# Kernel optimization log

Hardware: AMD Instinct MI355X
Metric: run time of the kernel (lower is better)

The kernel has to match this reference:

```python
import jax, jax.numpy as jnp
import numpy as np
from jax import lax

EPS = 1e-5

def silu(x):
    return x * jax.nn.sigmoid(x)

def rms_norm(x, w):
    return x * lax.rsqrt(jnp.mean(x * x, axis=-1, keepdims=True) + EPS) * w

def causal_dwconv(x, w, b):
    # x: (B, L, d), w: (d, K) depthwise causal conv, pad left K-1
    K = w.shape[1]
    L = x.shape[1]
    xp = jnp.pad(x, ((0, 0), (K - 1, 0), (0, 0)))
    y = sum(w[:, k] * xp[:, k:k + L, :] for k in range(K))
    return y + b

def selective_scan(xs_in, dt, Bm, Cm, A):
    # xs_in, dt: (B, L, d); Bm, Cm: (B, L, n); A: (d, n)
    Bsz, L, d = xs_in.shape
    n = A.shape[1]

    def step(h, inp):
        dt_t, B_t, C_t, x_t = inp  # (B,d),(B,n),(B,n),(B,d)
        dA = jnp.exp(dt_t[:, :, None] * A)            # (B,d,n)
        h = h * dA + (dt_t * x_t)[:, :, None] * B_t[:, None, :]
        y = jnp.einsum('bdn,bn->bd', h, C_t)
        return h, y

    xs = (jnp.swapaxes(dt, 0, 1), jnp.swapaxes(Bm, 0, 1),
          jnp.swapaxes(Cm, 0, 1), jnp.swapaxes(xs_in, 0, 1))
    h0 = jnp.zeros((Bsz, d, n), xs_in.dtype)
    _, ys = lax.scan(step, h0, xs)
    return jnp.swapaxes(ys, 0, 1)  # (B, L, d)

def mamba1(x, nw, ipw, cw, cb, xpw, dtw, dtb, Alog, Dp, opw):
    # Block: out = mixer(rmsnorm(x)); caller adds residual x.
    xn = rms_norm(x, nw)
    xz = xn @ ipw.T                      # (B,L,2d)
    d = ipw.shape[0] // 2
    xc, z = xz[..., :d], xz[..., d:]
    xc = silu(causal_dwconv(xc, cw, cb))
    dbl = xc @ xpw.T                     # (B,L,r+2n)
    r = dtw.shape[1]
    n = Alog.shape[1]
    dt = jax.nn.softplus(dbl[..., :r] @ dtw.T + dtb)  # (B,L,d)
    Bm = dbl[..., r:r + n]
    Cm = dbl[..., r + n:r + 2 * n]
    A = -jnp.exp(Alog)
    y = selective_scan(xc, dt, Bm, Cm, A)
    y = y + Dp * xc
    y = y * silu(z)
    return y @ opw.T

def mamba_bidir(x, P, i_f, i_b):
    # P: tuple of stacked param arrays; indices select direction-specific params
    (nw, ipw, cw, cb, xpw, dtw, dtb, Alog, Dp, opw) = P

    def m(xx, i):
        return mamba1(xx, nw[i], ipw[i], cw[i], cb[i], xpw[i],
                      dtw[i], dtb[i], Alog[i], Dp[i], opw[i])

    yf = x + m(x, i_f)
    xb = x[:, ::-1, :]
    yb = (xb + m(xb, i_b))[:, ::-1, :]
    return jnp.concatenate([yf, yb], axis=-1)  # (B, L, 2c)

def tf_mamba(x, norm_w, in_proj_w, conv_w, conv_b, x_proj_w, dt_proj_w,
             dt_proj_b, A_log, D, out_proj_w, tlin_w, tlin_b, flin_w, flin_b):
    b, c, t, f = x.shape
    P = (norm_w, in_proj_w, conv_w, conv_b, x_proj_w, dt_proj_w, dt_proj_b,
         A_log, D, out_proj_w)
    xt = jnp.transpose(x, (0, 3, 2, 1)).reshape(b * f, t, c)
    xt = mamba_bidir(xt, P, 0, 1) @ tlin_w + tlin_b + xt
    xf = xt.reshape(b, f, t, c).transpose(0, 2, 1, 3).reshape(b * t, f, c)
    xf = mamba_bidir(xf, P, 2, 3) @ flin_w + flin_b + xf
    return xf.reshape(b, t, f, c).transpose(0, 3, 1, 2)

def setup_inputs() -> dict:
    key = jax.random.key(0)
    b, c, t, f = 1, 64, 128, 128
    expand, n, K = 4, 16, 4
    d = expand * c            # 256
    r = (c + 15) // 16        # dt_rank = 4
    ks = jax.random.split(key, 12)
    f32 = jnp.float32

    # dt bias init as in Mamba: dt ~ exp(U(log 1e-3, log 0.1)); bias = softplus^-1(dt)
    dt = jnp.exp(jax.random.uniform(ks[0], (4, d)) *
                 (np.log(0.1) - np.log(0.001)) + np.log(0.001))
    dt_proj_b = dt + jnp.log(-jnp.expm1(-dt))

    inp = {
        'x': jax.random.normal(ks[1], (b, c, t, f), f32),
        'norm_w': jnp.ones((4, c), f32),
        'in_proj_w': jax.random.normal(ks[2], (4, 2 * d, c), f32) * 0.02,
        'conv_w': jax.random.normal(ks[3], (4, d, K), f32) * (1.0 / np.sqrt(K)),
        'conv_b': jnp.zeros((4, d), f32),
        'x_proj_w': jax.random.normal(ks[4], (4, r + 2 * n, d), f32) * 0.02,
        'dt_proj_w': jax.random.normal(ks[5], (4, d, r), f32) * (r ** -0.5),
        'dt_proj_b': dt_proj_b.astype(f32),
        'A_log': jnp.log(jnp.broadcast_to(
            jnp.arange(1, n + 1, dtype=f32), (4, d, n))).copy(),
        'D': jnp.ones((4, d), f32),
        'out_proj_w': jax.random.normal(ks[6], (4, c, d), f32) * 0.02,
        'tlin_w': jax.random.normal(ks[7], (2 * c, c), f32) * 0.02,
        'tlin_b': jnp.zeros((c,), f32),
        'flin_w': jax.random.normal(ks[8], (2 * c, c), f32) * 0.02,
        'flin_b': jnp.zeros((c,), f32),
    }
    return inp

def reference(x, norm_w, in_proj_w, conv_w, conv_b, x_proj_w, dt_proj_w,
              dt_proj_b, A_log, D, out_proj_w, tlin_w, tlin_b, flin_w, flin_b):
    return tf_mamba(x, norm_w, in_proj_w, conv_w, conv_b, x_proj_w, dt_proj_w,
                    dt_proj_b, A_log, D, out_proj_w, tlin_w, tlin_b, flin_w,
                    flin_b)
```

## Files before the change

kernel.cpp:

```cpp
#include <hip/hip_runtime.h>
#include <math.h>

#define LSEQ 128
#define NROW 128
#define POS (LSEQ*NROW)
#define CDIM 64
#define DDIM 256
#define NSTATE 16
#define RDIM 4
#define KCONV 4

__global__ __launch_bounds__(256) void k_prep1(const float* __restrict__ x,
                                               float* __restrict__ seq_in) {
    __shared__ float tile[64][65];
    int t   = blockIdx.x & 127;
    int fi0 = (blockIdx.x >> 7) << 6;
    int lane = threadIdx.x & 63;
    int r    = threadIdx.x >> 6;
    #pragma unroll
    for (int i = 0; i < 16; i++) {
        int cc = 4*i + r;
        tile[cc][lane] = x[cc*16384 + t*128 + fi0 + lane];
    }
    __syncthreads();
    #pragma unroll
    for (int i = 0; i < 16; i++) {
        int fl = 4*i + r;
        seq_in[(fi0 + fl)*8192 + t*64 + lane] = tile[lane][fl];
    }
}

__global__ __launch_bounds__(256) void k_final(const float* __restrict__ s,
                                               float* __restrict__ outp) {
    __shared__ float tile[64][65];
    int t   = blockIdx.x & 127;
    int fi0 = (blockIdx.x >> 7) << 6;
    int lane = threadIdx.x & 63;
    int r    = threadIdx.x >> 6;
    #pragma unroll
    for (int i = 0; i < 16; i++) {
        int fl = 4*i + r;
        tile[fl][lane] = s[(((t << 7) + fi0 + fl) << 6) + lane];
    }
    __syncthreads();
    #pragma unroll
    for (int i = 0; i < 16; i++) {
        int cc = 4*i + r;
        outp[cc*16384 + (t << 7) + fi0 + lane] = tile[lane][cc];
    }
}

__global__ __launch_bounds__(256) void k_rstd(const float* __restrict__ seq_in,
                                              float* __restrict__ rstd) {
    int p    = blockIdx.x*4 + (threadIdx.x >> 6);
    int lane = threadIdx.x & 63;
    float v = seq_in[p*64 + lane];
    float s = v*v;
    #pragma unroll
    for (int off = 32; off; off >>= 1) s += __shfl_xor(s, off, 64);
    if (lane == 0) rstd[p] = rsqrtf(s*(1.0f/64.0f) + 1e-5f);
}

__global__ __launch_bounds__(512) void k_inproj(const float* __restrict__ seq_in,
                                                const float* __restrict__ rstd,
                                                const float* __restrict__ nw_s,
                                                const float* __restrict__ ipw_s,
                                                float* __restrict__ xc_pre,
                                                float* __restrict__ zbuf) {
    __shared__ float xn[32][64];
    int dir = blockIdx.x >> 9;
    int g0  = (blockIdx.x & 511) << 5;
    size_t dirOff = (size_t)dir * POS * DDIM;
    const float* nw  = nw_s  + dir*CDIM;
    const float* ipw = ipw_s + (size_t)dir * 2*DDIM*CDIM;

    for (int i = threadIdx.x; i < 32*64; i += 512) {
        int pi = i >> 6, k = i & 63;
        int p = g0 + pi;
        int row = p >> 7, tau = p & 127;
        int s = dir ? (127 - tau) : tau;
        int q = (row << 7) + s;
        xn[pi][k] = seq_in[(q << 6) + k] * rstd[q] * nw[k];
    }
    __syncthreads();

    int j = threadIdx.x;
    const float4* w4 = (const float4*)(ipw + (j << 6));
    float acc[32];
    #pragma unroll
    for (int i = 0; i < 32; i++) acc[i] = 0.f;
    #pragma unroll
    for (int k4 = 0; k4 < 16; k4++) {
        float4 wv = w4[k4];
        #pragma unroll
        for (int i = 0; i < 32; i++) {
            float4 xv = *((const float4*)&xn[i][k4 << 2]);
            acc[i] += wv.x*xv.x + wv.y*xv.y + wv.z*xv.z + wv.w*xv.w;
        }
    }
    float* dst = (j < 256) ? (xc_pre + dirOff + j) : (zbuf + dirOff + (j - 256));
    #pragma unroll
    for (int i = 0; i < 32; i++) dst[(size_t)(g0 + i)*DDIM] = acc[i];
}

__global__ __launch_bounds__(256) void k_convxproj(const float* __restrict__ xc_pre,
                                                   const float* __restrict__ cw_s,
                                                   const float* __restrict__ cb_s,
                                                   const float* __restrict__ xpw_s,
                                                   const float* __restrict__ dtw_s,
                                                   const float* __restrict__ dtb_s,
                                                   float* __restrict__ xcb,
                                                   float* __restrict__ dtout,
                                                   float* __restrict__ bc) {
    __shared__ float lx[16][260];
    __shared__ float w[36][260];
    __shared__ float dbl[16][37];
    int dir = blockIdx.x >> 10;
    int g0  = (blockIdx.x & 1023) << 4;
    int tau0 = g0 & 127;
    size_t dirOff = (size_t)dir * POS * DDIM;
    const float* cw  = cw_s  + dir*DDIM*KCONV;
    const float* cb  = cb_s  + dir*DDIM;
    const float* xpw = xpw_s + (size_t)dir*36*DDIM;
    const float* dtw = dtw_s + dir*DDIM*RDIM;
    const float* dtb = dtb_s + dir*DDIM;
    int t = threadIdx.x;

    {
        const float4* src = (const float4*)xpw;
        for (int idx4 = t; idx4 < 36*64; idx4 += 256) {
            int j = idx4 >> 6, k4 = idx4 & 63;
            ((float4*)&w[j][0])[k4] = src[idx4];
        }
    }

    float r[19];
    #pragma unroll
    for (int j = 0; j < 19; j++) {
        r[j] = (tau0 == 0 && j < 3) ? 0.f
             : xc_pre[dirOff + (size_t)(g0 - 3 + j)*DDIM + t];
    }
    float c0 = cw[t*4], c1 = cw[t*4+1], c2 = cw[t*4+2], c3 = cw[t*4+3];
    float cbv = cb[t];
    #pragma unroll
    for (int i = 0; i < 16; i++) {
        float a = cbv + c0*r[i] + c1*r[i+1] + c2*r[i+2] + c3*r[i+3];
        float sv = a / (1.f + __expf(-a));
        lx[i][t] = sv;
        xcb[dirOff + (size_t)(g0 + i)*DDIM + t] = sv;
    }
    __syncthreads();

    #pragma unroll
    for (int rep = 0; rep < 3; rep++) {
        int oid = rep*256 + t;
        if (oid < 576) {
            int pos = oid & 15;
            int j   = oid >> 4;
            const float4* xr = (const float4*)&lx[pos][0];
            const float4* wr = (const float4*)&w[j][0];
            float a0 = 0.f, a1 = 0.f, a2 = 0.f, a3 = 0.f;
            #pragma unroll 4
            for (int k4 = 0; k4 < 64; k4 += 4) {
                float4 x0 = xr[k4],   w0 = wr[k4];
                float4 x1 = xr[k4+1], w1 = wr[k4+1];
                float4 x2 = xr[k4+2], w2 = wr[k4+2];
                float4 x3 = xr[k4+3], w3 = wr[k4+3];
                a0 += x0.x*w0.x + x0.y*w0.y + x0.z*w0.z + x0.w*w0.w;
                a1 += x1.x*w1.x + x1.y*w1.y + x1.z*w1.z + x1.w*w1.w;
                a2 += x2.x*w2.x + x2.y*w2.y + x2.z*w2.z + x2.w*w2.w;
                a3 += x3.x*w3.x + x3.y*w3.y + x3.z*w3.z + x3.w*w3.w;
            }
            dbl[pos][j] = (a0 + a1) + (a2 + a3);
        }
    }
    __syncthreads();

    float dbv = dtb[t];
    float w0 = dtw[t*4], w1 = dtw[t*4+1], w2 = dtw[t*4+2], w3 = dtw[t*4+3];
    #pragma unroll
    for (int i = 0; i < 16; i++) {
        float a = dbv + dbl[i][0]*w0 + dbl[i][1]*w1 + dbl[i][2]*w2 + dbl[i][3]*w3;
        float sp = (a > 0.f) ? (a + log1pf(__expf(-a))) : log1pf(__expf(a));
        dtout[dirOff + (size_t)(g0 + i)*DDIM + t] = sp;
    }
    #pragma unroll
    for (int rep = 0; rep < 2; rep++) {
        int idx = rep*256 + t;
        int pos = idx >> 5, jj = idx & 31;
        bc[(size_t)dir*POS*32 + (size_t)(g0 + pos)*32 + jj] = dbl[pos][4 + jj];
    }
}

__global__ __launch_bounds__(256) void k_scan(const float* __restrict__ xc,
                                              const float* __restrict__ dt,
                                              const float* __restrict__ bc,
                                              const float* __restrict__ Alog_s,
                                              const float* __restrict__ Dp_s,
                                              const float* __restrict__ zbuf,
                                              float* __restrict__ y) {
    __shared__ float sBC[128*32];
    int dir = blockIdx.x >> 7;
    int row = blockIdx.x & 127;
    int ch  = threadIdx.x;
    size_t dirOff = (size_t)dir * POS * DDIM;
    const float* Alog = Alog_s + dir*DDIM*NSTATE;
    const float* Dp   = Dp_s   + dir*DDIM;

    for (int i = threadIdx.x; i < 128*32; i += 256)
        sBC[i] = bc[(size_t)dir*POS*32 + (size_t)row*4096 + i];
    float a[16], h[16];
    #pragma unroll
    for (int i = 0; i < 16; i++) {
        a[i] = -__expf(Alog[ch*16 + i]);
        h[i] = 0.f;
    }
    float dv = Dp[ch];
    __syncthreads();

    size_t off = dirOff + ((size_t)row*128)*DDIM + ch;
    float dtv = dt[off], xv = xc[off], zv = zbuf[off];
    const size_t ybase = dirOff + ((size_t)row << 7)*DDIM + ch;
    for (int tau = 0; tau < 128; tau++) {
        float dtn = 0.f, xn_ = 0.f, zn = 0.f;
        if (tau < 127) {
            size_t offn = off + DDIM;
            dtn = dt[offn]; xn_ = xc[offn]; zn = zbuf[offn];
        }
        float dtx = dtv*xv;
        const float* B = &sBC[tau*32];
        float ac0 = 0.f, ac1 = 0.f, ac2 = 0.f, ac3 = 0.f;
        #pragma unroll
        for (int i = 0; i < 16; i += 4) {
            float dA0 = __expf(dtv*a[i]);
            float dA1 = __expf(dtv*a[i+1]);
            float dA2 = __expf(dtv*a[i+2]);
            float dA3 = __expf(dtv*a[i+3]);
            h[i]   = h[i]*dA0   + dtx*B[i];
            h[i+1] = h[i+1]*dA1 + dtx*B[i+1];
            h[i+2] = h[i+2]*dA2 + dtx*B[i+2];
            h[i+3] = h[i+3]*dA3 + dtx*B[i+3];
            ac0 += h[i]*B[16+i];
            ac1 += h[i+1]*B[16+i+1];
            ac2 += h[i+2]*B[16+i+2];
            ac3 += h[i+3]*B[16+i+3];
        }
        float yv = (ac0 + ac1) + (ac2 + ac3) + dv*xv;
        yv *= zv / (1.f + __expf(-zv));
        int s = dir ? (127 - tau) : tau;
        y[ybase + (size_t)s*DDIM] = yv;
        dtv = dtn; xv = xn_; zv = zn; off += DDIM;
    }
}

__global__ __launch_bounds__(256) void k_outlin(const float* __restrict__ y,
                                                const float* __restrict__ opw_s,
                                                const float* __restrict__ seq_in,
                                                const float* __restrict__ lw,
                                                const float* __restrict__ lb,
                                                float* __restrict__ seq_out,
                                                int twrite) {
    __shared__ float ly0[16][256];
    __shared__ float ly1[16][256];
    __shared__ float si[16][64];
    __shared__ float cat[16][128];
    int g0 = blockIdx.x << 4;
    for (int i = threadIdx.x; i < 16*256; i += 256) {
        ly0[i >> 8][i & 255] = y[((size_t)g0 << 8) + i];
        ly1[i >> 8][i & 255] = y[(size_t)POS*DDIM + ((size_t)g0 << 8) + i];
    }
    for (int i = threadIdx.x; i < 16*64; i += 256)
        si[i >> 6][i & 63] = seq_in[((size_t)g0 << 6) + i];
    __syncthreads();

    int cc  = threadIdx.x & 63;
    int sub = threadIdx.x >> 6;
    const float4* wf = (const float4*)(opw_s + (cc << 8));
    const float4* wb = (const float4*)(opw_s + CDIM*DDIM + (cc << 8));
    float accf[4] = {0.f,0.f,0.f,0.f};
    float accb[4] = {0.f,0.f,0.f,0.f};
    for (int k4 = 0; k4 < 64; k4++) {
        float4 wvf = wf[k4];
        float4 wvb = wb[k4];
        #pragma unroll
        for (int ii = 0; ii < 4; ii++) {
            int i = (sub << 2) + ii;
            float4 xf = *((const float4*)&ly0[i][k4 << 2]);
            float4 xb = *((const float4*)&ly1[i][k4 << 2]);
            accf[ii] += wvf.x*xf.x + wvf.y*xf.y + wvf.z*xf.z + wvf.w*xf.w;
            accb[ii] += wvb.x*xb.x + wvb.y*xb.y + wvb.z*xb.z + wvb.w*xb.w;
        }
    }
    #pragma unroll
    for (int ii = 0; ii < 4; ii++) {
        int i = (sub << 2) + ii;
        cat[i][cc]      = si[i][cc] + accf[ii];
        cat[i][64 + cc] = si[i][cc] + accb[ii];
    }
    __syncthreads();

    float accl[4];
    float bv = lb[cc];
    #pragma unroll
    for (int ii = 0; ii < 4; ii++) accl[ii] = bv;
    for (int k = 0; k < 128; k++) {
        float w = lw[k*64 + cc];
        #pragma unroll
        for (int ii = 0; ii < 4; ii++) accl[ii] += cat[(sub << 2) + ii][k]*w;
    }
    #pragma unroll
    for (int ii = 0; ii < 4; ii++) {
        int i = (sub << 2) + ii;
        int p = g0 + i;
        float v = accl[ii] + si[i][cc];
        if (twrite) {
            int dstp = ((p & 127) << 7) + (p >> 7);
            seq_out[((size_t)dstp << 6) + cc] = v;
        } else {
            seq_out[((size_t)p << 6) + cc] = v;
        }
    }
}

extern "C" void kernel_launch(void* const* d_in, const int* in_sizes, int n_in,
                              void* d_out, int out_size, void* d_ws, size_t ws_size,
                              hipStream_t stream) {
    (void)in_sizes; (void)n_in; (void)out_size; (void)ws_size;
    const float* x      = (const float*)d_in[0];
    const float* norm_w = (const float*)d_in[1];
    const float* ipw    = (const float*)d_in[2];
    const float* cw     = (const float*)d_in[3];
    const float* cb     = (const float*)d_in[4];
    const float* xpw    = (const float*)d_in[5];
    const float* dtw    = (const float*)d_in[6];
    const float* dtbp   = (const float*)d_in[7];
    const float* Alog   = (const float*)d_in[8];
    const float* Dp     = (const float*)d_in[9];
    const float* opw    = (const float*)d_in[10];
    const float* tlw    = (const float*)d_in[11];
    const float* tlb    = (const float*)d_in[12];
    const float* flw    = (const float*)d_in[13];
    const float* flb    = (const float*)d_in[14];
    float* outp = (float*)d_out;

    float* ws       = (float*)d_ws;
    float* seq_in   = ws;
    float* rstd     = seq_in  + (size_t)POS*64;
    float* xc_pre   = rstd    + POS;
    float* zbuf     = xc_pre  + (size_t)2*POS*256;
    float* xcb      = zbuf    + (size_t)2*POS*256;
    float* dtbuf    = xcb     + (size_t)2*POS*256;
    float* bc       = dtbuf   + (size_t)2*POS*256;
    float* seq_out  = bc      + (size_t)2*POS*32;

    auto stage = [&](int st, const float* lw, const float* lb, int twrite,
                     float* sout) {
        int pi = 2*st;
        k_rstd     <<<POS/4, 256, 0, stream>>>(seq_in, rstd);
        k_inproj   <<<2*POS/32, 512, 0, stream>>>(seq_in, rstd,
                        norm_w + pi*CDIM, ipw + (size_t)pi*2*DDIM*CDIM,
                        xc_pre, zbuf);
        k_convxproj<<<2*POS/16, 256, 0, stream>>>(xc_pre,
                        cw + pi*DDIM*KCONV, cb + pi*DDIM,
                        xpw + (size_t)pi*36*DDIM,
                        dtw + pi*DDIM*RDIM, dtbp + pi*DDIM,
                        xcb, dtbuf, bc);
        k_scan     <<<2*NROW, 256, 0, stream>>>(xcb, dtbuf, bc,
                        Alog + (size_t)pi*DDIM*NSTATE, Dp + pi*DDIM,
                        zbuf, xc_pre);
        k_outlin   <<<POS/16, 256, 0, stream>>>(xc_pre,
                        opw + (size_t)pi*CDIM*DDIM, seq_in, lw, lb,
                        sout, twrite);
    };

    k_prep1<<<256, 256, 0, stream>>>(x, seq_in);
    stage(0, tlw, tlb, 1, seq_out);

    {
        float* tmp = seq_in; seq_in = seq_out; seq_out = tmp;
    }
    stage(1, flw, flb, 0, seq_out);

    k_final<<<256, 256, 0, stream>>>(seq_out, outp);
}
```

Measured before the change: 620.4 us.

## Fuse rmsnorm into inproj, move dt projection into scan, retile projections

The separate rstd kernel is removed and the RMS norm is computed inside the input projection, which now uses 128-thread blocks over 16 positions with four weight rows per thread. The conv/x_proj kernel no longer stages weights in shared memory. It writes the raw 36-wide dbl vector, and the scan kernel computes dt (projection plus softplus) on the fly, prefetching two steps ahead. This removes the full d-wide dt buffer round-trip. The output/linear kernel is retiled so each thread computes a 2x2 block of outputs. In exchange, the scan's serial loop does more arithmetic per step, and weights are read directly from global memory.

```diff
diff --git a/kernel.cpp b/kernel.cpp
--- a/kernel.cpp
+++ b/kernel.cpp
@@ -10,6 +10,10 @@
 #define RDIM 4
 #define KCONV 4
 
+static __forceinline__ __device__ float dot4(float4 a, float4 b) {
+    return a.x*b.x + a.y*b.y + a.z*b.z + a.w*b.w;
+}
+
 __global__ __launch_bounds__(256) void k_prep1(const float* __restrict__ x,
                                                float* __restrict__ seq_in) {
     __shared__ float tile[64][65];
@@ -50,71 +54,73 @@
     }
 }
 
-__global__ __launch_bounds__(256) void k_rstd(const float* __restrict__ seq_in,
-                                              float* __restrict__ rstd) {
-    int p    = blockIdx.x*4 + (threadIdx.x >> 6);
-    int lane = threadIdx.x & 63;
-    float v = seq_in[p*64 + lane];
-    float s = v*v;
-    #pragma unroll
-    for (int off = 32; off; off >>= 1) s += __shfl_xor(s, off, 64);
-    if (lane == 0) rstd[p] = rsqrtf(s*(1.0f/64.0f) + 1e-5f);
-}
-
-__global__ __launch_bounds__(512) void k_inproj(const float* __restrict__ seq_in,
-                                                const float* __restrict__ rstd,
+__global__ __launch_bounds__(128) void k_inproj(const float* __restrict__ seq_in,
                                                 const float* __restrict__ nw_s,
                                                 const float* __restrict__ ipw_s,
                                                 float* __restrict__ xc_pre,
                                                 float* __restrict__ zbuf) {
-    __shared__ float xn[32][64];
-    int dir = blockIdx.x >> 9;
-    int g0  = (blockIdx.x & 511) << 5;
+    __shared__ float xn[16][64];
+    int dir = blockIdx.x >> 10;
+    int g0  = (blockIdx.x & 1023) << 4;
     size_t dirOff = (size_t)dir * POS * DDIM;
     const float* nw  = nw_s  + dir*CDIM;
     const float* ipw = ipw_s + (size_t)dir * 2*DDIM*CDIM;
 
-    for (int i = threadIdx.x; i < 32*64; i += 512) {
-        int pi = i >> 6, k = i & 63;
+    int wv   = threadIdx.x >> 6;
+    int lane = threadIdx.x & 63;
+    float nwv = nw[lane];
+    #pragma unroll
+    for (int pi = wv; pi < 16; pi += 2) {
         int p = g0 + pi;
         int row = p >> 7, tau = p & 127;
         int s = dir ? (127 - tau) : tau;
         int q = (row << 7) + s;
-        xn[pi][k] = seq_in[(q << 6) + k] * rstd[q] * nw[k];
+        float v = seq_in[(q << 6) + lane];
+        float ss = v*v;
+        #pragma unroll
+        for (int off = 32; off; off >>= 1) ss += __shfl_xor(ss, off, 64);
+        float rs = rsqrtf(ss*(1.0f/64.0f) + 1e-5f);
+        xn[pi][lane] = v*rs*nwv;
     }
     __syncthreads();
 
     int j = threadIdx.x;
-    const float4* w4 = (const float4*)(ipw + (j << 6));
-    float acc[32];
-    #pragma unroll
-    for (int i = 0; i < 32; i++) acc[i] = 0.f;
-    #pragma unroll
+    const float4* w0p = (const float4*)(ipw + (j << 6));
+    const float4* w1p = (const float4*)(ipw + ((j + 128) << 6));
+    const float4* w2p = (const float4*)(ipw + ((j + 256) << 6));
+    const float4* w3p = (const float4*)(ipw + ((j + 384) << 6));
+    float acc0[16], acc1[16], acc2[16], acc3[16];
+    #pragma unroll
+    for (int i = 0; i < 16; i++) { acc0[i] = 0.f; acc1[i] = 0.f; acc2[i] = 0.f; acc3[i] = 0.f; }
+    #pragma unroll 4
     for (int k4 = 0; k4 < 16; k4++) {
-        float4 wv = w4[k4];
+        float4 wa = w0p[k4], wb = w1p[k4], wc = w2p[k4], wd = w3p[k4];
         #pragma unroll
-        for (int i = 0; i < 32; i++) {
+        for (int i = 0; i < 16; i++) {
             float4 xv = *((const float4*)&xn[i][k4 << 2]);
-            acc[i] += wv.x*xv.x + wv.y*xv.y + wv.z*xv.z + wv.w*xv.w;
-        }
-    }
-    float* dst = (j < 256) ? (xc_pre + dirOff + j) : (zbuf + dirOff + (j - 256));
-    #pragma unroll
-    for (int i = 0; i < 32; i++) dst[(size_t)(g0 + i)*DDIM] = acc[i];
+            acc0[i] += dot4(wa, xv);
+            acc1[i] += dot4(wb, xv);
+            acc2[i] += dot4(wc, xv);
+            acc3[i] += dot4(wd, xv);
+        }
+    }
+    #pragma unroll
+    for (int i = 0; i < 16; i++) {
+        size_t base = dirOff + (size_t)(g0 + i)*DDIM;
+        xc_pre[base + j]       = acc0[i];
+        xc_pre[base + j + 128] = acc1[i];
+        zbuf  [base + j]       = acc2[i];
+        zbuf  [base + j + 128] = acc3[i];
+    }
 }
 
 __global__ __launch_bounds__(256) void k_convxproj(const float* __restrict__ xc_pre,
                                                    const float* __restrict__ cw_s,
                                                    const float* __restrict__ cb_s,
                                                    const float* __restrict__ xpw_s,
-                                                   const float* __restrict__ dtw_s,
-                                                   const float* __restrict__ dtb_s,
                                                    float* __restrict__ xcb,
-                                                   float* __restrict__ dtout,
-                                                   float* __restrict__ bc) {
+                                                   float* __restrict__ dblg) {
     __shared__ float lx[16][260];
-    __shared__ float w[36][260];
-    __shared__ float dbl[16][37];
     int dir = blockIdx.x >> 10;
     int g0  = (blockIdx.x & 1023) << 4;
     int tau0 = g0 & 127;
@@ -122,17 +128,7 @@
     const float* cw  = cw_s  + dir*DDIM*KCONV;
     const float* cb  = cb_s  + dir*DDIM;
     const float* xpw = xpw_s + (size_t)dir*36*DDIM;
-    const float* dtw = dtw_s + dir*DDIM*RDIM;
-    const float* dtb = dtb_s + dir*DDIM;
     int t = threadIdx.x;
-
-    {
-        const float4* src = (const float4*)xpw;
-        for (int idx4 = t; idx4 < 36*64; idx4 += 256) {
-            int j = idx4 >> 6, k4 = idx4 & 63;
-            ((float4*)&w[j][0])[k4] = src[idx4];
-        }
-    }
 
     float r[19];
     #pragma unroll
@@ -158,57 +154,49 @@
             int pos = oid & 15;
             int j   = oid >> 4;
             const float4* xr = (const float4*)&lx[pos][0];
-            const float4* wr = (const float4*)&w[j][0];
+            const float4* wr = (const float4*)(xpw + (j << 8));
             float a0 = 0.f, a1 = 0.f, a2 = 0.f, a3 = 0.f;
             #pragma unroll 4
             for (int k4 = 0; k4 < 64; k4 += 4) {
-                float4 x0 = xr[k4],   w0 = wr[k4];
-                float4 x1 = xr[k4+1], w1 = wr[k4+1];
-                float4 x2 = xr[k4+2], w2 = wr[k4+2];
-                float4 x3 = xr[k4+3], w3 = wr[k4+3];
-                a0 += x0.x*w0.x + x0.y*w0.y + x0.z*w0.z + x0.w*w0.w;
-                a1 += x1.x*w1.x + x1.y*w1.y + x1.z*w1.z + x1.w*w1.w;
-                a2 += x2.x*w2.x + x2.y*w2.y + x2.z*w2.z + x2.w*w2.w;
-                a3 += x3.x*w3.x + x3.y*w3.y + x3.z*w3.z + x3.w*w3.w;
+                float4 xv0 = xr[k4],   wv0 = wr[k4];
+                float4 xv1 = xr[k4+1], wv1 = wr[k4+1];
+                float4 xv2 = xr[k4+2], wv2 = wr[k4+2];
+                float4 xv3 = xr[k4+3], wv3 = wr[k4+3];
+                a0 += dot4(wv0, xv0);
+                a1 += dot4(wv1, xv1);
+                a2 += dot4(wv2, xv2);
+                a3 += dot4(wv3, xv3);
             }
-            dbl[pos][j] = (a0 + a1) + (a2 + a3);
-        }
-    }
-    __syncthreads();
-
-    float dbv = dtb[t];
-    float w0 = dtw[t*4], w1 = dtw[t*4+1], w2 = dtw[t*4+2], w3 = dtw[t*4+3];
-    #pragma unroll
-    for (int i = 0; i < 16; i++) {
-        float a = dbv + dbl[i][0]*w0 + dbl[i][1]*w1 + dbl[i][2]*w2 + dbl[i][3]*w3;
-        float sp = (a > 0.f) ? (a + log1pf(__expf(-a))) : log1pf(__expf(a));
-        dtout[dirOff + (size_t)(g0 + i)*DDIM + t] = sp;
-    }
-    #pragma unroll
-    for (int rep = 0; rep < 2; rep++) {
-        int idx = rep*256 + t;
-        int pos = idx >> 5, jj = idx & 31;
-        bc[(size_t)dir*POS*32 + (size_t)(g0 + pos)*32 + jj] = dbl[pos][4 + jj];
+            dblg[(size_t)dir*POS*36 + (size_t)(g0 + pos)*36 + j] =
+                (a0 + a1) + (a2 + a3);
+        }
     }
 }
 
 __global__ __launch_bounds__(256) void k_scan(const float* __restrict__ xc,
-                                              const float* __restrict__ dt,
-                                              const float* __restrict__ bc,
+                                              const float* __restrict__ dblg,
+                                              const float* __restrict__ dtw_s,
+                                              const float* __restrict__ dtb_s,
                                               const float* __restrict__ Alog_s,
                                               const float* __restrict__ Dp_s,
                                               const float* __restrict__ zbuf,
                                               float* __restrict__ y) {
-    __shared__ float sBC[128*32];
+    __shared__ float sdbl[128*36];
     int dir = blockIdx.x >> 7;
     int row = blockIdx.x & 127;
     int ch  = threadIdx.x;
     size_t dirOff = (size_t)dir * POS * DDIM;
     const float* Alog = Alog_s + dir*DDIM*NSTATE;
     const float* Dp   = Dp_s   + dir*DDIM;
-
-    for (int i = threadIdx.x; i < 128*32; i += 256)
-        sBC[i] = bc[(size_t)dir*POS*32 + (size_t)row*4096 + i];
+    const float* dtw  = dtw_s  + dir*DDIM*RDIM;
+    const float* dtb  = dtb_s  + dir*DDIM;
+
+    {
+        const float4* src = (const float4*)(dblg + (size_t)dir*POS*36
+                                            + (size_t)row*128*36);
+        float4* dst = (float4*)sdbl;
+        for (int i = threadIdx.x; i < 128*36/4; i += 256) dst[i] = src[i];
+    }
     float a[16], h[16];
     #pragma unroll
     for (int i = 0; i < 16; i++) {
@@ -216,19 +204,27 @@
         h[i] = 0.f;
     }
     float dv = Dp[ch];
+    float tw0 = dtw[ch*4], tw1 = dtw[ch*4+1], tw2 = dtw[ch*4+2], tw3 = dtw[ch*4+3];
+    float tb  = dtb[ch];
     __syncthreads();
 
     size_t off = dirOff + ((size_t)row*128)*DDIM + ch;
-    float dtv = dt[off], xv = xc[off], zv = zbuf[off];
-    const size_t ybase = dirOff + ((size_t)row << 7)*DDIM + ch;
+    const size_t ybase = off;
+    float x0 = xc[off],        z0 = zbuf[off];
+    float x1 = xc[off + DDIM], z1 = zbuf[off + DDIM];
     for (int tau = 0; tau < 128; tau++) {
-        float dtn = 0.f, xn_ = 0.f, zn = 0.f;
-        if (tau < 127) {
-            size_t offn = off + DDIM;
-            dtn = dt[offn]; xn_ = xc[offn]; zn = zbuf[offn];
-        }
-        float dtx = dtv*xv;
-        const float* B = &sBC[tau*32];
+        float x2 = 0.f, z2 = 0.f;
+        if (tau + 2 < 128) {
+            size_t offn = off + 2*DDIM;
+            x2 = xc[offn]; z2 = zbuf[offn];
+        }
+        const float* db = &sdbl[tau*36];
+        float adt = tb + db[0]*tw0 + db[1]*tw1 + db[2]*tw2 + db[3]*tw3;
+        float dtv = (adt > 0.f) ? (adt + log1pf(__expf(-adt)))
+                                : log1pf(__expf(adt));
+        float dtx = dtv*x0;
+        const float* B = db + 4;
+        const float* C = db + 20;
         float ac0 = 0.f, ac1 = 0.f, ac2 = 0.f, ac3 = 0.f;
         #pragma unroll
         for (int i = 0; i < 16; i += 4) {
@@ -240,16 +236,16 @@
             h[i+1] = h[i+1]*dA1 + dtx*B[i+1];
             h[i+2] = h[i+2]*dA2 + dtx*B[i+2];
             h[i+3] = h[i+3]*dA3 + dtx*B[i+3];
-            ac0 += h[i]*B[16+i];
-            ac1 += h[i+1]*B[16+i+1];
-            ac2 += h[i+2]*B[16+i+2];
-            ac3 += h[i+3]*B[16+i+3];
-        }
-        float yv = (ac0 + ac1) + (ac2 + ac3) + dv*xv;
-        yv *= zv / (1.f + __expf(-zv));
+            ac0 += h[i]*C[i];
+            ac1 += h[i+1]*C[i+1];
+            ac2 += h[i+2]*C[i+2];
+            ac3 += h[i+3]*C[i+3];
+        }
+        float yv = (ac0 + ac1) + (ac2 + ac3) + dv*x0;
+        yv *= z0 / (1.f + __expf(-z0));
         int s = dir ? (127 - tau) : tau;
         y[ybase + (size_t)s*DDIM] = yv;
-        dtv = dtn; xv = xn_; zv = zn; off += DDIM;
+        x0 = x1; z0 = z1; x1 = x2; z1 = z2; off += DDIM;
     }
 }
 
@@ -273,51 +269,64 @@
         si[i >> 6][i & 63] = seq_in[((size_t)g0 << 6) + i];
     __syncthreads();
 
-    int cc  = threadIdx.x & 63;
-    int sub = threadIdx.x >> 6;
-    const float4* wf = (const float4*)(opw_s + (cc << 8));
-    const float4* wb = (const float4*)(opw_s + CDIM*DDIM + (cc << 8));
-    float accf[4] = {0.f,0.f,0.f,0.f};
-    float accb[4] = {0.f,0.f,0.f,0.f};
+    int cc  = threadIdx.x & 31;
+    int sub = threadIdx.x >> 5;
+    int i0 = sub << 1, i1 = i0 + 1;
+    const float4* wf0 = (const float4*)(opw_s + (cc << 8));
+    const float4* wf1 = (const float4*)(opw_s + ((cc + 32) << 8));
+    const float4* wb0 = (const float4*)(opw_s + CDIM*DDIM + (cc << 8));
+    const float4* wb1 = (const float4*)(opw_s + CDIM*DDIM + ((cc + 32) << 8));
+    float f00 = 0.f, f01 = 0.f, f10 = 0.f, f11 = 0.f;
+    float b00 = 0.f, b01 = 0.f, b10 = 0.f, b11 = 0.f;
     for (int k4 = 0; k4 < 64; k4++) {
-        float4 wvf = wf[k4];
-        float4 wvb = wb[k4];
-        #pragma unroll
-        for (int ii = 0; ii < 4; ii++) {
-            int i = (sub << 2) + ii;
-            float4 xf = *((const float4*)&ly0[i][k4 << 2]);
-            float4 xb = *((const float4*)&ly1[i][k4 << 2]);
-            accf[ii] += wvf.x*xf.x + wvf.y*xf.y + wvf.z*xf.z + wvf.w*xf.w;
-            accb[ii] += wvb.x*xb.x + wvb.y*xb.y + wvb.z*xb.z + wvb.w*xb.w;
-        }
-    }
-    #pragma unroll
-    for (int ii = 0; ii < 4; ii++) {
-        int i = (sub << 2) + ii;
-        cat[i][cc]      = si[i][cc] + accf[ii];
-        cat[i][64 + cc] = si[i][cc] + accb[ii];
-    }
-    __syncthreads();
-
-    float accl[4];
-    float bv = lb[cc];
-    #pragma unroll
-    for (int ii = 0; ii < 4; ii++) accl[ii] = bv;
-    for (int k = 0; k < 128; k++) {
-        float w = lw[k*64 + cc];
-        #pragma unroll
-        for (int ii = 0; ii < 4; ii++) accl[ii] += cat[(sub << 2) + ii][k]*w;
-    }
-    #pragma unroll
-    for (int ii = 0; ii < 4; ii++) {
-        int i = (sub << 2) + ii;
+        float4 xf0 = *((const float4*)&ly0[i0][k4 << 2]);
+        float4 xf1 = *((const float4*)&ly0[i1][k4 << 2]);
+        float4 xb0 = *((const float4*)&ly1[i0][k4 << 2]);
+        float4 xb1 = *((const float4*)&ly1[i1][k4 << 2]);
+        float4 wa = wf0[k4], wb = wf1[k4], wc = wb0[k4], wd = wb1[k4];
+        f00 += dot4(wa, xf0);  f10 += dot4(wa, xf1);
+        f01 += dot4(wb, xf0);  f11 += dot4(wb, xf1);
+        b00 += dot4(wc, xb0);  b10 += dot4(wc, xb1);
+        b01 += dot4(wd, xb0);  b11 += dot4(wd, xb1);
+    }
+    cat[i0][cc]           = si[i0][cc]      + f00;
+    cat[i1][cc]           = si[i1][cc]      + f10;
+    cat[i0][cc + 32]      = si[i0][cc + 32] + f01;
+    cat[i1][cc + 32]      = si[i1][cc + 32] + f11;
+    cat[i0][64 + cc]      = si[i0][cc]      + b00;
+    cat[i1][64 + cc]      = si[i1][cc]      + b10;
+    cat[i0][64 + cc + 32] = si[i0][cc + 32] + b01;
+    cat[i1][64 + cc + 32] = si[i1][cc + 32] + b11;
+    __syncthreads();
+
+    float a00 = lb[cc], a01 = lb[cc + 32];
+    float a10 = a00,    a11 = a01;
+    for (int k4 = 0; k4 < 32; k4++) {
+        int k = k4 << 2;
+        float4 cA = *((const float4*)&cat[i0][k]);
+        float4 cB = *((const float4*)&cat[i1][k]);
+        const float* lr = lw + (size_t)k*64;
+        float wA0 = lr[cc],       wA1 = lr[cc + 32];
+        float wB0 = lr[64 + cc],  wB1 = lr[64 + cc + 32];
+        float wC0 = lr[128 + cc], wC1 = lr[128 + cc + 32];
+        float wD0 = lr[192 + cc], wD1 = lr[192 + cc + 32];
+        a00 += cA.x*wA0 + cA.y*wB0 + cA.z*wC0 + cA.w*wD0;
+        a01 += cA.x*wA1 + cA.y*wB1 + cA.z*wC1 + cA.w*wD1;
+        a10 += cB.x*wA0 + cB.y*wB0 + cB.z*wC0 + cB.w*wD0;
+        a11 += cB.x*wA1 + cB.y*wB1 + cB.z*wC1 + cB.w*wD1;
+    }
+    #pragma unroll
+    for (int v = 0; v < 4; v++) {
+        int i  = (v & 1) ? i1 : i0;
+        int c  = (v & 2) ? (cc + 32) : cc;
+        float val = ((v == 0) ? a00 : (v == 1) ? a10 : (v == 2) ? a01 : a11)
+                    + si[i][c];
         int p = g0 + i;
-        float v = accl[ii] + si[i][cc];
         if (twrite) {
             int dstp = ((p & 127) << 7) + (p >> 7);
-            seq_out[((size_t)dstp << 6) + cc] = v;
+            seq_out[((size_t)dstp << 6) + c] = val;
         } else {
-            seq_out[((size_t)p << 6) + cc] = v;
+            seq_out[((size_t)p << 6) + c] = val;
         }
     }
 }
@@ -345,27 +354,24 @@
 
     float* ws       = (float*)d_ws;
     float* seq_in   = ws;
-    float* rstd     = seq_in  + (size_t)POS*64;
-    float* xc_pre   = rstd    + POS;
+    float* xc_pre   = seq_in  + (size_t)POS*64;
     float* zbuf     = xc_pre  + (size_t)2*POS*256;
     float* xcb      = zbuf    + (size_t)2*POS*256;
-    float* dtbuf    = xcb     + (size_t)2*POS*256;
-    float* bc       = dtbuf   + (size_t)2*POS*256;
-    float* seq_out  = bc      + (size_t)2*POS*32;
+    float* dblbuf   = xcb     + (size_t)2*POS*256;
+    float* seq_out  = dblbuf  + (size_t)2*POS*36;
 
     auto stage = [&](int st, const float* lw, const float* lb, int twrite,
                      float* sout) {
         int pi = 2*st;
-        k_rstd     <<<POS/4, 256, 0, stream>>>(seq_in, rstd);
-        k_inproj   <<<2*POS/32, 512, 0, stream>>>(seq_in, rstd,
+        k_inproj   <<<2*POS/16, 128, 0, stream>>>(seq_in,
                         norm_w + pi*CDIM, ipw + (size_t)pi*2*DDIM*CDIM,
                         xc_pre, zbuf);
         k_convxproj<<<2*POS/16, 256, 0, stream>>>(xc_pre,
                         cw + pi*DDIM*KCONV, cb + pi*DDIM,
                         xpw + (size_t)pi*36*DDIM,
+                        xcb, dblbuf);
+        k_scan     <<<2*NROW, 256, 0, stream>>>(xcb, dblbuf,
                         dtw + pi*DDIM*RDIM, dtbp + pi*DDIM,
-                        xcb, dtbuf, bc);
-        k_scan     <<<2*NROW, 256, 0, stream>>>(xcb, dtbuf, bc,
                         Alog + (size_t)pi*DDIM*NSTATE, Dp + pi*DDIM,
                         zbuf, xc_pre);
         k_outlin   <<<POS/16, 256, 0, stream>>>(xc_pre,
```

After: 783.8 us. 1.26x slower.
